# Performance work log

Measured on AMD Instinct MI355X. Metric: run time of the kernel, lower is better.

Reference implementation:

```python
import jax, jax.numpy as jnp
import numpy as np

G = 128          # density grid resolution (args.density_res)
MINN = -15.0     # self.minn_pts
EXTENT = 40.0    # self.maxx_pts - self.minn_pts
P_MASS = 1.0     # args.p_mass


def _p2g(act_xs, act_deform):
    """Quadratic B-spline point-to-grid scatter (MPM P2G), 3x3x3 neighbors.
    act_xs:     [T, N, 3] float particle positions
    act_deform: [T, N, 3] float per-particle deformation vectors
    Returns (grids [T,G,G,G], grid_deformation [T,G,G,G,3]).
    """
    T, N, _ = act_xs.shape
    Xp = (act_xs - MINN) / EXTENT * G                      # [T,N,3] grid-space coords
    base = jnp.floor(Xp - 0.5).astype(jnp.int32)           # [T,N,3]
    fx = Xp - base.astype(Xp.dtype)                        # [T,N,3], in [0.5, 1.5)
    # quadratic B-spline weights, one triple per axis: [3, T, N, 3]
    w = jnp.stack([0.5 * (1.5 - fx) ** 2,
                   0.75 - (fx - 1.0) ** 2,
                   0.5 * (fx - 0.5) ** 2], axis=0)
    # all 27 neighbor offsets
    offs = jnp.stack(jnp.meshgrid(jnp.arange(3), jnp.arange(3), jnp.arange(3),
                                  indexing='ij'), axis=-1).reshape(27, 3)
    # separable trilinear-style weight product: [27, T, N]
    weight = w[offs[:, 0], :, :, 0] * w[offs[:, 1], :, :, 1] * w[offs[:, 2], :, :, 2]
    base_c = jnp.clip(base, 0, G - 3)                      # keep 3x3x3 stencil in-bounds
    idx = base_c[None] + offs[:, None, None, :]            # [27,T,N,3]
    t_idx = jnp.arange(T, dtype=jnp.int32)[None, :, None]  # [1,T,1]
    flat = ((t_idx * G + idx[..., 0]) * G + idx[..., 1]) * G + idx[..., 2]  # [27,T,N]
    flat = flat.reshape(-1)
    grids = (jnp.zeros((T * G * G * G,), act_xs.dtype)
             .at[flat].add((weight * P_MASS).reshape(-1))
             .reshape(T, G, G, G))
    vals = weight[..., None] * act_deform[None]            # [27,T,N,3]
    gdef = (jnp.zeros((T * G * G * G, 3), act_xs.dtype)
            .at[flat].add(vals.reshape(-1, 3))
            .reshape(T, G, G, G, 3))
    return grids, gdef


def setup_inputs() -> dict:
    key = jax.random.key(0)
    k1, k2 = jax.random.split(key)
    T, N = 8, 100000
    # positions safely inside [minn+2, maxx-2] so the 3x3x3 stencil stays in-bounds
    act_xs = MINN + 2.0 + (EXTENT - 4.0) * jax.random.uniform(k1, (T, N, 3), dtype=jnp.float32)
    act_xs_deformation = 0.01 * jax.random.normal(k2, (T, N, 3), dtype=jnp.float32)
    return {"act_xs": act_xs, "act_xs_deformation": act_xs_deformation}


def reference(act_xs, act_xs_deformation):
    return _p2g(act_xs, act_xs_deformation)
```

## Files before the change

kernel.cpp:

```cpp
#include <hip/hip_runtime.h>


constexpr int   G       = 128;
constexpr int   CELLS   = G * G * G;
constexpr int   BUCKETS = CELLS / 4;
constexpr float MINN    = -15.0f;
constexpr float EXTENT  = 40.0f;

__device__ __forceinline__ int3 base_cell(float x, float y, float z,
                                          float& fx, float& fy, float& fz)
{
    const float scale = (float)G / EXTENT;
    const float Xp = (x - MINN) * scale;
    const float Yp = (y - MINN) * scale;
    const float Zp = (z - MINN) * scale;
    int bx = (int)floorf(Xp - 0.5f);
    int by = (int)floorf(Yp - 0.5f);
    int bz = (int)floorf(Zp - 0.5f);
    fx = Xp - (float)bx; fy = Yp - (float)by; fz = Zp - (float)bz;
    bx = min(max(bx, 0), G - 3);
    by = min(max(by, 0), G - 3);
    bz = min(max(bz, 0), G - 3);
    return make_int3(bx, by, bz);
}

__device__ __forceinline__ float wsel(float f, int d)
{
    const float r0 = 1.5f - f, r1 = f - 1.0f, r2 = f - 0.5f;
    const float w0 = 0.5f * r0 * r0;
    const float w1 = 0.75f - r1 * r1;
    const float w2 = 0.5f * r2 * r2;
    return d == 0 ? w0 : (d == 1 ? w1 : w2);
}

__global__ void __launch_bounds__(256)
cell_hist(const float* __restrict__ xs, int* __restrict__ arr, int N)
{
    const int p = blockIdx.x * blockDim.x + threadIdx.x;
    const int t = blockIdx.y;
    if (p >= N) return;
    const long i = (long)t * N + p;
    float fx, fy, fz;
    int3 b = base_cell(xs[i*3], xs[i*3+1], xs[i*3+2], fx, fy, fz);
    const int bucket = (b.x << 12) + (b.y << 5) + (b.z >> 2);
    atomicAdd(&arr[(long)t * BUCKETS + bucket], 1);
}

__global__ void __launch_bounds__(256)
scan1(int* __restrict__ arr, int* __restrict__ sums)
{
    const int t = blockIdx.y, tid = threadIdx.x;
    int* a = arr + (long)t * BUCKETS + (long)blockIdx.x * 4096 + tid * 16;
    int local[16], s = 0;
    #pragma unroll
    for (int i = 0; i < 16; ++i) { const int v = a[i]; local[i] = s; s += v; }
    __shared__ int part[256];
    part[tid] = s;
    __syncthreads();
    const int own = s;
    for (int d = 1; d < 256; d <<= 1) {
        int v = (tid >= d) ? part[tid - d] : 0;
        __syncthreads();
        part[tid] += v;
        __syncthreads();
    }
    const int excl = part[tid] - own;
    #pragma unroll
    for (int i = 0; i < 16; ++i) a[i] = excl + local[i];
    if (tid == 255) sums[t * 128 + blockIdx.x] = part[255];
}

__global__ void __launch_bounds__(128)
scan2(int* __restrict__ sums)
{
    const int t = blockIdx.x, tid = threadIdx.x;
    const int v = sums[t * 128 + tid];
    __shared__ int part[128];
    part[tid] = v;
    __syncthreads();
    for (int d = 1; d < 128; d <<= 1) {
        int u = (tid >= d) ? part[tid - d] : 0;
        __syncthreads();
        part[tid] += u;
        __syncthreads();
    }
    sums[t * 128 + tid] = part[tid] - v;
}

__global__ void __launch_bounds__(256)
scatter_cells(const float* __restrict__ xs, const float* __restrict__ def,
              int* __restrict__ arr, const int* __restrict__ sums,
              float4* __restrict__ sA, float2* __restrict__ sB, int N)
{
    const int p = blockIdx.x * blockDim.x + threadIdx.x;
    const int t = blockIdx.y;
    if (p >= N) return;
    const long i = (long)t * N + p;
    const float x = xs[i*3], y = xs[i*3+1], z = xs[i*3+2];
    float fx, fy, fz;
    int3 b = base_cell(x, y, z, fx, fy, fz);
    const float Zp = (z - MINN) * ((float)G / EXTENT);
    const int bucket = (b.x << 12) + (b.y << 5) + (b.z >> 2);
    const int slot = atomicAdd(&arr[(long)t * BUCKETS + bucket], 1)
                   + sums[t * 128 + (bucket >> 12)];
    const long o = (long)t * N + slot;
    sA[o] = make_float4(fx, fy, Zp, def[i*3]);
    sB[o] = make_float2(def[i*3+1], def[i*3+2]);
}

__global__ void __launch_bounds__(256)
gather_cells7(const float4* __restrict__ sA, const float2* __restrict__ sB,
              const int* __restrict__ arr, const int* __restrict__ sums,
              float* __restrict__ grids, float* __restrict__ gdef, int N)
{
    const int wid  = threadIdx.x >> 6;
    const int lane = threadIdx.x & 63;
    const int g    = lane >> 4;
    const int zl   = lane & 15;
    const int t = blockIdx.y;
    const int W = blockIdx.x * 4 + wid;
    const int col = W >> 1;
    const int zbase = (W & 1) << 6;
    const int cy = col & (G - 1);
    const int cx = col >> 7;
    const int cz = zbase + lane;

    __shared__ int2   descBC[4][4][9];
    __shared__ float4 rec[4][4][17];
    __shared__ float  ws[4][3][4][17];

    const int* a  = arr + (long)t * BUCKETS;
    const int* sm = sums + t * 128;
    const long pbase = (long)t * N;

    if (lane < 36) {
        const int g2 = lane / 9;
        const int r2 = lane - 9 * g2;
        const int rx = cx - 2 + r2 / 3;
        const int ry = cy - 2 + r2 % 3;
        int beg = 0, cnt = 0;
        if (rx >= 0 && ry >= 0) {
            const int rb = (rx << 12) + (ry << 5);
            const int bb = (zbase >> 2) + (g2 << 2);
            const int c1 = rb + bb + 3;
            const int e  = a[c1] + sm[c1 >> 12];
            const int c0 = rb + bb - 2;
            beg = (c0 >= 0) ? (a[c0] + sm[c0 >> 12]) : 0;
            cnt = max(e - beg, 0);
        }
        descBC[wid][g2][r2] = make_int2(beg, cnt);
    }

    const int2 d0_ = descBC[wid][g][0], d1_ = descBC[wid][g][1],
               d2_ = descBC[wid][g][2], d3_ = descBC[wid][g][3],
               d4_ = descBC[wid][g][4], d5_ = descBC[wid][g][5],
               d6_ = descBC[wid][g][6], d7_ = descBC[wid][g][7],
               d8_ = descBC[wid][g][8];
    const int p1 = d0_.y;
    const int p2 = p1 + d1_.y;
    const int p3 = p2 + d2_.y;
    const int p4 = p3 + d3_.y;
    const int p5 = p4 + d4_.y;
    const int p6 = p5 + d5_.y;
    const int p7 = p6 + d6_.y;
    const int p8 = p7 + d7_.y;
    const int tot = p8 + d8_.y;
    const int adj0 = d0_.x;
    const int adj1 = d1_.x - p1;
    const int adj2 = d2_.x - p2;
    const int adj3 = d3_.x - p3;
    const int adj4 = d4_.x - p4;
    const int adj5 = d5_.x - p5;
    const int adj6 = d6_.x - p6;
    const int adj7 = d7_.x - p7;
    const int adj8 = d8_.x - p8;

    int mt = max(tot, __shfl_xor(tot, 16));
    mt = max(mt, __shfl_xor(mt, 32));

    float m = 0.f, v0 = 0.f, v1 = 0.f, v2 = 0.f;

    for (int p0 = 0; p0 < mt; p0 += 16) {
        const int j = p0 + zl;
        if (j < tot) {
            const int g1_ = (j >= p1), g2_ = (j >= p2), g3_ = (j >= p3),
                      g4_ = (j >= p4), g5_ = (j >= p5), g6_ = (j >= p6),
                      g7_ = (j >= p7), g8_ = (j >= p8);
            int ad = adj0;
            ad = g1_ ? adj1 : ad;  ad = g2_ ? adj2 : ad;  ad = g3_ ? adj3 : ad;
            ad = g4_ ? adj4 : ad;  ad = g5_ ? adj5 : ad;  ad = g6_ ? adj6 : ad;
            ad = g7_ ? adj7 : ad;  ad = g8_ ? adj8 : ad;
            const int dp = 10 - g1_ - g2_ - 2*g3_ - g4_ - g5_ - 2*g6_ - g7_ - g8_;
            const int idx = j + ad;

            const float4 A = sA[pbase + idx];
            const float2 B = sB[pbase + idx];
            const float bzf = floorf(A.z - 0.5f);
            const float fz  = A.z - bzf;
            const float wxy = wsel(A.x, dp >> 2) * wsel(A.y, dp & 3);
            const float q0 = 1.5f - fz, q1 = fz - 1.0f, q2 = fz - 0.5f;
            rec[wid][g][zl] =
                make_float4(__int_as_float((int)bzf), A.w, B.x, B.y);
            ws[wid][0][g][zl] = wxy * (0.5f * q0 * q0);
            ws[wid][1][g][zl] = wxy * (0.75f - q1 * q1);
            ws[wid][2][g][zl] = wxy * (0.5f * q2 * q2);
        }
        const int cc = min(tot - p0, 16);
        for (int p = 0; p < cc; ++p) {
            const float4 R  = rec[wid][g][p];
            const float w0 = ws[wid][0][g][p];
            const float w1 = ws[wid][1][g][p];
            const float w2 = ws[wid][2][g][p];
            const int k = cz - __float_as_int(R.x);
            float w = (k == 0) ? w0 : 0.0f;
            w = (k == 1) ? w1 : w;
            w = (k == 2) ? w2 : w;
            m  += w;
            v0 += w * R.y;
            v1 += w * R.z;
            v2 += w * R.w;
        }
    }

    const long gidx = (long)t * CELLS + ((long)col << 7) + cz;
    grids[gidx]      = m;
    gdef[gidx*3 + 0] = v0;
    gdef[gidx*3 + 1] = v1;
    gdef[gidx*3 + 2] = v2;
}

__global__ void __launch_bounds__(256)
p2g_direct(const float* __restrict__ xs, const float* __restrict__ def,
           float* __restrict__ grids, float* __restrict__ gdef, int N)
{
    const int p = blockIdx.x * blockDim.x + threadIdx.x;
    const int t = blockIdx.y;
    if (p >= N) return;
    const long i = (long)t * N + p;
    const float dx = def[i*3], dy = def[i*3+1], dz = def[i*3+2];
    float fx, fy, fz;
    int3 b = base_cell(xs[i*3], xs[i*3+1], xs[i*3+2], fx, fy, fz);
    float wx[3], wy[3], wz[3];
    wx[0] = 0.5f*(1.5f-fx)*(1.5f-fx); wx[1] = 0.75f-(fx-1.f)*(fx-1.f); wx[2] = 0.5f*(fx-0.5f)*(fx-0.5f);
    wy[0] = 0.5f*(1.5f-fy)*(1.5f-fy); wy[1] = 0.75f-(fy-1.f)*(fy-1.f); wy[2] = 0.5f*(fy-0.5f)*(fy-0.5f);
    wz[0] = 0.5f*(1.5f-fz)*(1.5f-fz); wz[1] = 0.75f-(fz-1.f)*(fz-1.f); wz[2] = 0.5f*(fz-0.5f)*(fz-0.5f);
    const long tbase = (long)t * CELLS;
    #pragma unroll
    for (int ii = 0; ii < 3; ++ii) {
        const long xoff = tbase + (long)(b.x + ii) * (G * G);
        #pragma unroll
        for (int jj = 0; jj < 3; ++jj) {
            const float wij = wx[ii] * wy[jj];
            const long yoff = xoff + (long)(b.y + jj) * G;
            #pragma unroll
            for (int kk = 0; kk < 3; ++kk) {
                const float w = wij * wz[kk];
                const long idx = yoff + (b.z + kk);
                atomicAdd(&grids[idx], w);
                atomicAdd(&gdef[idx*3+0], w * dx);
                atomicAdd(&gdef[idx*3+1], w * dy);
                atomicAdd(&gdef[idx*3+2], w * dz);
            }
        }
    }
}

extern "C" void kernel_launch(void* const* d_in, const int* in_sizes, int n_in,
                              void* d_out, int out_size, void* d_ws, size_t ws_size,
                              hipStream_t stream)
{
    const float* xs  = (const float*)d_in[0];
    const float* def = (const float*)d_in[1];
    float* out = (float*)d_out;

    const int T = (int)(out_size / ((long)CELLS * 4));
    const int N = in_sizes[0] / (3 * T);

    float* grids = out;
    float* gdef  = out + (long)T * CELLS;

    const size_t szA    = (size_t)T * N * sizeof(float4);
    const size_t szB    = (size_t)T * N * sizeof(float2);
    const size_t szArr  = (size_t)T * BUCKETS * sizeof(int);
    const size_t szSums = (size_t)T * 128 * sizeof(int);
    const size_t need   = szA + szB + szArr + szSums;

    if (ws_size >= need) {
        char* ws = (char*)d_ws;
        float4* sA   = (float4*)ws;  ws += szA;
        float2* sB   = (float2*)ws;  ws += szB;
        int*    arr  = (int*)ws;     ws += szArr;
        int*    sums = (int*)ws;

        hipMemsetAsync(arr, 0, szArr, stream);

        dim3 pgrid((N + 255) / 256, T);
        cell_hist    <<<pgrid, dim3(256), 0, stream>>>(xs, arr, N);
        scan1        <<<dim3(BUCKETS / 4096, T), dim3(256), 0, stream>>>(arr, sums);
        scan2        <<<dim3(T), dim3(128), 0, stream>>>(sums);
        scatter_cells<<<pgrid, dim3(256), 0, stream>>>(xs, def, arr, sums, sA, sB, N);
        gather_cells7<<<dim3(CELLS / 256, T), dim3(256), 0, stream>>>(
            sA, sB, arr, sums, grids, gdef, N);
        return;
    }

    hipMemsetAsync(d_out, 0, (size_t)out_size * sizeof(float), stream);
    dim3 grid((N + 255) / 256, T);
    p2g_direct<<<grid, dim3(256), 0, stream>>>(xs, def, grids, gdef, N);
}
```

Before: 251.9 us.

## Gather a full z-column per wave with two cells per lane

The gather kernel now gives each wave a whole 128-cell z-column instead of half a column. Each lane accumulates two cells, at z and z+16 within its 32-z group. The lane's 4-lane group now covers a 32-z slab (8 buckets plus halo), so each particle record loaded from shared memory feeds two cells. This amortises the neighbor-bucket reads and the halo-overlap particles that two half-column waves used to fetch twice. In exchange it launches half as many waves, doubles the accumulator registers, and lengthens the per-wave loops.

```diff
diff --git a/kernel.cpp b/kernel.cpp
--- a/kernel.cpp
+++ b/kernel.cpp
@@ -109,21 +109,20 @@
 }
 
 __global__ void __launch_bounds__(256)
-gather_cells7(const float4* __restrict__ sA, const float2* __restrict__ sB,
-              const int* __restrict__ arr, const int* __restrict__ sums,
-              float* __restrict__ grids, float* __restrict__ gdef, int N)
+gather_col(const float4* __restrict__ sA, const float2* __restrict__ sB,
+           const int* __restrict__ arr, const int* __restrict__ sums,
+           float* __restrict__ grids, float* __restrict__ gdef, int N)
 {
     const int wid  = threadIdx.x >> 6;
     const int lane = threadIdx.x & 63;
     const int g    = lane >> 4;
     const int zl   = lane & 15;
     const int t = blockIdx.y;
-    const int W = blockIdx.x * 4 + wid;
-    const int col = W >> 1;
-    const int zbase = (W & 1) << 6;
+    const int col = blockIdx.x * 4 + wid;
     const int cy = col & (G - 1);
     const int cx = col >> 7;
-    const int cz = zbase + lane;
+    const int cza = (g << 5) + zl;
+    const int czb = cza + 16;
 
     __shared__ int2   descBC[4][4][9];
     __shared__ float4 rec[4][4][17];
@@ -141,8 +140,8 @@
         int beg = 0, cnt = 0;
         if (rx >= 0 && ry >= 0) {
             const int rb = (rx << 12) + (ry << 5);
-            const int bb = (zbase >> 2) + (g2 << 2);
-            const int c1 = rb + bb + 3;
+            const int bb = g2 << 3;
+            const int c1 = rb + bb + 7;
             const int e  = a[c1] + sm[c1 >> 12];
             const int c0 = rb + bb - 2;
             beg = (c0 >= 0) ? (a[c0] + sm[c0 >> 12]) : 0;
@@ -178,7 +177,8 @@
     int mt = max(tot, __shfl_xor(tot, 16));
     mt = max(mt, __shfl_xor(mt, 32));
 
-    float m = 0.f, v0 = 0.f, v1 = 0.f, v2 = 0.f;
+    float ma = 0.f, va0 = 0.f, va1 = 0.f, va2 = 0.f;
+    float mb = 0.f, vb0 = 0.f, vb1 = 0.f, vb2 = 0.f;
 
     for (int p0 = 0; p0 < mt; p0 += 16) {
         const int j = p0 + zl;
@@ -211,22 +211,27 @@
             const float w0 = ws[wid][0][g][p];
             const float w1 = ws[wid][1][g][p];
             const float w2 = ws[wid][2][g][p];
-            const int k = cz - __float_as_int(R.x);
-            float w = (k == 0) ? w0 : 0.0f;
-            w = (k == 1) ? w1 : w;
-            w = (k == 2) ? w2 : w;
-            m  += w;
-            v0 += w * R.y;
-            v1 += w * R.z;
-            v2 += w * R.w;
+            const int bz = __float_as_int(R.x);
+            const int ka = cza - bz;
+            const int kb = czb - bz;
+            float wa = (ka == 0) ? w0 : 0.0f;
+            wa = (ka == 1) ? w1 : wa;
+            wa = (ka == 2) ? w2 : wa;
+            float wb = (kb == 0) ? w0 : 0.0f;
+            wb = (kb == 1) ? w1 : wb;
+            wb = (kb == 2) ? w2 : wb;
+            ma += wa;  va0 += wa * R.y;  va1 += wa * R.z;  va2 += wa * R.w;
+            mb += wb;  vb0 += wb * R.y;  vb1 += wb * R.z;  vb2 += wb * R.w;
         }
     }
 
-    const long gidx = (long)t * CELLS + ((long)col << 7) + cz;
-    grids[gidx]      = m;
-    gdef[gidx*3 + 0] = v0;
-    gdef[gidx*3 + 1] = v1;
-    gdef[gidx*3 + 2] = v2;
+    const long cbase = (long)t * CELLS + ((long)col << 7);
+    const long ga = cbase + cza;
+    const long gb = cbase + czb;
+    grids[ga] = ma;
+    grids[gb] = mb;
+    gdef[ga*3 + 0] = va0;  gdef[ga*3 + 1] = va1;  gdef[ga*3 + 2] = va2;
+    gdef[gb*3 + 0] = vb0;  gdef[gb*3 + 1] = vb1;  gdef[gb*3 + 2] = vb2;
 }
 
 __global__ void __launch_bounds__(256)
@@ -299,7 +304,7 @@
         scan1        <<<dim3(BUCKETS / 4096, T), dim3(256), 0, stream>>>(arr, sums);
         scan2        <<<dim3(T), dim3(128), 0, stream>>>(sums);
         scatter_cells<<<pgrid, dim3(256), 0, stream>>>(xs, def, arr, sums, sA, sB, N);
-        gather_cells7<<<dim3(CELLS / 256, T), dim3(256), 0, stream>>>(
+        gather_col   <<<dim3(G * G / 4, T), dim3(256), 0, stream>>>(
             sA, sB, arr, sums, grids, gdef, N);
         return;
     }
```

Measured after the change: 257.1 us. 2.1% more time.
